# Optimization experiments

Hardware: AMD Instinct MI355X
Metric: run time of the kernel (lower is better)

The kernel has to match this reference:

```python
import jax, jax.numpy as jnp
import numpy as np


def setup_inputs() -> dict:
    key = jax.random.key(0)
    k1, k2 = jax.random.split(key)
    B, T = 8192, 1024
    confidences = jax.random.uniform(k1, (B, T), dtype=jnp.float32)
    accuracies = jax.random.bernoulli(k2, 0.5, (B, T)).astype(jnp.float32)
    return {"confidences": confidences, "accuracies": accuracies}


def reference(confidences, accuracies):
    # exclusive cumulative product of (1 - conf): prod_{s<t} (1 - conf[:, s])
    no_buzz = 1.0 - confidences                      # [B, T]
    cum = jnp.cumprod(no_buzz, axis=1)               # inclusive cumprod
    excl = jnp.concatenate([jnp.ones_like(cum[:, :1]), cum[:, :-1]], axis=1)
    buzz_probs = confidences * excl                  # [B, T]
    system_scores = jnp.sum(buzz_probs * accuracies, axis=1)   # [B]
    correction = 1.0 - jnp.sum(buzz_probs, axis=1)             # [B]
    system_scores = system_scores + correction * accuracies[:, -1]
    return -jnp.mean(system_scores)
```

## Files before the change

kernel.cpp:

```cpp
#include <hip/hip_runtime.h>


#define TLEN 1024
#define CHUNK 16
#define WAVES_PER_BLOCK 16

__global__ __launch_bounds__(1024)
void buzz_loss_kernel(const float* __restrict__ conf,
                      const float* __restrict__ acc,
                      float* __restrict__ out,
                      float neg_inv_b) {
    const int lane = threadIdx.x & 63;
    const int wave = threadIdx.x >> 6;
    const long long row = (long long)blockIdx.x * WAVES_PER_BLOCK + wave;

    const float* cp = conf + row * TLEN + lane * CHUNK;
    const float* ap = acc  + row * TLEN + lane * CHUNK;

    float4 cv[4], av[4];
    #pragma unroll
    for (int j = 0; j < 4; ++j) {
        cv[j] = ((const float4*)cp)[j];
        av[j] = ((const float4*)ap)[j];
    }
    float c[CHUNK], a[CHUNK];
    #pragma unroll
    for (int j = 0; j < 4; ++j) {
        c[4*j+0] = cv[j].x; c[4*j+1] = cv[j].y; c[4*j+2] = cv[j].z; c[4*j+3] = cv[j].w;
        a[4*j+0] = av[j].x; a[4*j+1] = av[j].y; a[4*j+2] = av[j].z; a[4*j+3] = av[j].w;
    }

    float p = 1.0f;
    #pragma unroll
    for (int k = 0; k < CHUNK; ++k) p *= (1.0f - c[k]);

    float incl = p;
    #pragma unroll
    for (int off = 1; off < 64; off <<= 1) {
        float v = __shfl_up(incl, off, 64);
        if (lane >= off) incl *= v;
    }
    float prefix = __shfl_up(incl, 1, 64);
    if (lane == 0) prefix = 1.0f;

    float run = prefix;
    float sba = 0.0f, sb = 0.0f;
    #pragma unroll
    for (int k = 0; k < CHUNK; ++k) {
        float b = c[k] * run;
        sba += b * a[k];
        sb  += b;
        run *= (1.0f - c[k]);
    }

    float alast = __shfl(a[CHUNK - 1], 63, 64);

    #pragma unroll
    for (int off = 32; off; off >>= 1) {
        sba += __shfl_xor(sba, off, 64);
        sb  += __shfl_xor(sb,  off, 64);
    }

    float score = sba + (1.0f - sb) * alast;

    __shared__ float smem[WAVES_PER_BLOCK];
    if (lane == 0) smem[wave] = score;
    __syncthreads();
    if (threadIdx.x == 0) {
        float s = 0.0f;
        #pragma unroll
        for (int w = 0; w < WAVES_PER_BLOCK; ++w) s += smem[w];
        atomicAdd(out, s * neg_inv_b);
    }
}

extern "C" void kernel_launch(void* const* d_in, const int* in_sizes, int n_in,
                              void* d_out, int out_size, void* d_ws, size_t ws_size,
                              hipStream_t stream) {
    const float* conf = (const float*)d_in[0];
    const float* acc  = (const float*)d_in[1];
    float* out = (float*)d_out;

    const int total = in_sizes[0];
    const int B = total / TLEN;
    const int blocks = B / WAVES_PER_BLOCK;

    hipMemsetAsync(d_out, 0, sizeof(float), stream);

    buzz_loss_kernel<<<blocks, 64 * WAVES_PER_BLOCK, 0, stream>>>(
        conf, acc, out, -1.0f / (float)B);
}
```

Measured before the change: 95.06 us.

## Coalesce row loads into four segments and replace atomics with two-stage reduction

Each wave now reads its row as four contiguous 256-element segments, so lanes load adjacent float4 values and every load is fully coalesced instead of each lane reading a strided 16-float chunk. This costs four wave-level prefix scans per row instead of one, with the running product carried between segments. The final atomicAdd and the memset are replaced by a per-block partial write plus a single-block reduce kernel. That removes atomic contention and makes the sum deterministic, but adds a second kernel launch.

```diff
diff --git a/kernel.cpp b/kernel.cpp
--- a/kernel.cpp
+++ b/kernel.cpp
@@ -2,65 +2,67 @@
 
 
 #define TLEN 1024
-#define CHUNK 16
+#define NSEG 4
+#define SEGW 256
 #define WAVES_PER_BLOCK 16
 
 __global__ __launch_bounds__(1024)
-void buzz_loss_kernel(const float* __restrict__ conf,
-                      const float* __restrict__ acc,
-                      float* __restrict__ out,
-                      float neg_inv_b) {
+void buzz_loss_partial(const float* __restrict__ conf,
+                       const float* __restrict__ acc,
+                       float* __restrict__ partial) {
     const int lane = threadIdx.x & 63;
     const int wave = threadIdx.x >> 6;
     const long long row = (long long)blockIdx.x * WAVES_PER_BLOCK + wave;
 
-    const float* cp = conf + row * TLEN + lane * CHUNK;
-    const float* ap = acc  + row * TLEN + lane * CHUNK;
+    const float* crow = conf + row * TLEN;
+    const float* arow = acc  + row * TLEN;
 
-    float4 cv[4], av[4];
+    float4 cv[NSEG], av[NSEG];
     #pragma unroll
-    for (int j = 0; j < 4; ++j) {
-        cv[j] = ((const float4*)cp)[j];
-        av[j] = ((const float4*)ap)[j];
-    }
-    float c[CHUNK], a[CHUNK];
-    #pragma unroll
-    for (int j = 0; j < 4; ++j) {
-        c[4*j+0] = cv[j].x; c[4*j+1] = cv[j].y; c[4*j+2] = cv[j].z; c[4*j+3] = cv[j].w;
-        a[4*j+0] = av[j].x; a[4*j+1] = av[j].y; a[4*j+2] = av[j].z; a[4*j+3] = av[j].w;
+    for (int s = 0; s < NSEG; ++s) {
+        cv[s] = ((const float4*)(crow + s * SEGW))[lane];
+        av[s] = ((const float4*)(arow + s * SEGW))[lane];
     }
 
-    float p = 1.0f;
+    float carry = 1.0f;
+    float sba = 0.0f, sb = 0.0f;
+    float alast = 0.0f;
+
     #pragma unroll
-    for (int k = 0; k < CHUNK; ++k) p *= (1.0f - c[k]);
+    for (int s = 0; s < NSEG; ++s) {
+        float c[4] = {cv[s].x, cv[s].y, cv[s].z, cv[s].w};
+        float a[4] = {av[s].x, av[s].y, av[s].z, av[s].w};
 
-    float incl = p;
-    #pragma unroll
-    for (int off = 1; off < 64; off <<= 1) {
-        float v = __shfl_up(incl, off, 64);
-        if (lane >= off) incl *= v;
+        float p = (1.0f - c[0]) * (1.0f - c[1]) * (1.0f - c[2]) * (1.0f - c[3]);
+
+        float incl = p;
+        #pragma unroll
+        for (int off = 1; off < 64; off <<= 1) {
+            float v = __shfl_up(incl, off, 64);
+            if (lane >= off) incl *= v;
+        }
+        float prefix = __shfl_up(incl, 1, 64);
+        if (lane == 0) prefix = 1.0f;
+        float run = carry * prefix;
+
+        #pragma unroll
+        for (int k = 0; k < 4; ++k) {
+            float b = c[k] * run;
+            sba += b * a[k];
+            sb  += b;
+            run *= (1.0f - c[k]);
+        }
+
+        carry *= __shfl(incl, 63, 64);
+
+        if (s == NSEG - 1) alast = __shfl(a[3], 63, 64);
     }
-    float prefix = __shfl_up(incl, 1, 64);
-    if (lane == 0) prefix = 1.0f;
-
-    float run = prefix;
-    float sba = 0.0f, sb = 0.0f;
-    #pragma unroll
-    for (int k = 0; k < CHUNK; ++k) {
-        float b = c[k] * run;
-        sba += b * a[k];
-        sb  += b;
-        run *= (1.0f - c[k]);
-    }
-
-    float alast = __shfl(a[CHUNK - 1], 63, 64);
 
     #pragma unroll
     for (int off = 32; off; off >>= 1) {
         sba += __shfl_xor(sba, off, 64);
         sb  += __shfl_xor(sb,  off, 64);
     }
-
     float score = sba + (1.0f - sb) * alast;
 
     __shared__ float smem[WAVES_PER_BLOCK];
@@ -70,7 +72,25 @@
         float s = 0.0f;
         #pragma unroll
         for (int w = 0; w < WAVES_PER_BLOCK; ++w) s += smem[w];
-        atomicAdd(out, s * neg_inv_b);
+        partial[blockIdx.x] = s;
+    }
+}
+
+__global__ __launch_bounds__(512)
+void buzz_loss_reduce(const float* __restrict__ partial, float* __restrict__ out,
+                      float neg_inv_b, int n) {
+    const int tid = threadIdx.x;
+    float v = (tid < n) ? partial[tid] : 0.0f;
+    #pragma unroll
+    for (int off = 32; off; off >>= 1) v += __shfl_xor(v, off, 64);
+    __shared__ float smem[8];
+    if ((tid & 63) == 0) smem[tid >> 6] = v;
+    __syncthreads();
+    if (tid == 0) {
+        float s = 0.0f;
+        #pragma unroll
+        for (int w = 0; w < 8; ++w) s += smem[w];
+        out[0] = s * neg_inv_b;
     }
 }
 
@@ -80,13 +100,12 @@
     const float* conf = (const float*)d_in[0];
     const float* acc  = (const float*)d_in[1];
     float* out = (float*)d_out;
+    float* partial = (float*)d_ws;
 
     const int total = in_sizes[0];
     const int B = total / TLEN;
     const int blocks = B / WAVES_PER_BLOCK;
 
-    hipMemsetAsync(d_out, 0, sizeof(float), stream);
-
-    buzz_loss_kernel<<<blocks, 64 * WAVES_PER_BLOCK, 0, stream>>>(
-        conf, acc, out, -1.0f / (float)B);
+    buzz_loss_partial<<<blocks, 64 * WAVES_PER_BLOCK, 0, stream>>>(conf, acc, partial);
+    buzz_loss_reduce<<<1, 512, 0, stream>>>(partial, out, -1.0f / (float)B, blocks);
 }
```

Result: faster. 91.11 us (-4.1%).
